# Kernel tuning notes

Measured on AMD Instinct MI355X. Metric: run time of the kernel, lower is better.

The kernel has to match this reference:

```python
import jax, jax.numpy as jnp
import numpy as np

ISIZE, REC, NACT, BS = 512, 1024, 18, 64
CLIPVAL = 2.0

def setup_inputs() -> dict:
    key = jax.random.key(0)
    ks = jax.random.split(key, 12)
    return {
        "inputs": jax.random.normal(ks[0], (BS, ISIZE), jnp.float32),
        "recurrent_vals": jax.random.normal(ks[1], (BS, REC), jnp.float32),
        "hebb": jax.random.normal(ks[2], (BS, REC, REC), jnp.float32) * 0.1,
        # plastic params
        "w": 0.001 * jax.random.uniform(ks[3], (REC, REC), jnp.float32),
        "alpha": 0.001 * jax.random.uniform(ks[4], (REC, REC), jnp.float32),
        # layer 0: Linear(isize, rec)
        "W0": jax.random.normal(ks[5], (REC, ISIZE), jnp.float32) / np.sqrt(ISIZE),
        "b0": jnp.zeros((REC,), jnp.float32),
        # layer 1: Linear(rec, NBACTIONS)
        "W1": jax.random.normal(ks[6], (NACT, REC), jnp.float32) / np.sqrt(REC),
        "b1": jnp.zeros((NACT,), jnp.float32),
        # h2mod: Linear(rec, 1)
        "h2mod_w": jax.random.normal(ks[7], (1, REC), jnp.float32) / np.sqrt(REC),
        "h2mod_b": jnp.zeros((1,), jnp.float32),
        # modfanout: Linear(1, rec)
        "modfanout_w": jax.random.normal(ks[8], (REC, 1), jnp.float32),
        "modfanout_b": jnp.zeros((REC,), jnp.float32),
    }


def reference(inputs, recurrent_vals, hebb, w, alpha, W0, b0, W1, b1,
              h2mod_w, h2mod_b, modfanout_w, modfanout_b):
    # recurrent layer (i == rec_layer_in == 0):
    # tanh(Linear0(x) + rv @ (w + alpha*hebb))  with per-batch plastic weights
    plastic = w[None, :, :] + alpha[None, :, :] * hebb          # [b, rec, rec]
    rec_in = jnp.einsum('bi,bij->bj', recurrent_vals, plastic)  # [b, rec]
    hactiv = jnp.tanh(inputs @ W0.T + b0 + rec_in)              # [b, rec]
    rec_layer_values = hactiv                                   # i == rec_layer_out
    logits = hactiv @ W1.T + b1                                 # [b, nact]
    act_dis = jax.nn.softmax(logits, axis=1)                    # sf=True
    # neuromodulation
    myeta = jnp.tanh(rec_layer_values @ h2mod_w.T + h2mod_b)    # [b, 1]
    eta = myeta[:, :, None] * modfanout_w.reshape(1, 1, REC) + modfanout_b  # [b,1,rec]
    deltahebb = recurrent_vals[:, :, None] * rec_layer_values[:, None, :]   # [b,rec,rec]
    hebb_return = jnp.clip(hebb + eta * deltahebb, -CLIPVAL, CLIPVAL)
    return act_dis, rec_layer_values, hebb_return
```

## Files before the change

### kernel.cpp

```cpp
#include <hip/hip_runtime.h>
#include <cmath>

constexpr int ISIZE = 512;
constexpr int REC   = 1024;
constexpr int NACT  = 18;
constexpr int BS    = 64;
constexpr float CLIPVAL = 2.0f;

constexpr int NSLOT = 17;


typedef float f4 __attribute__((ext_vector_type(4)));

__device__ __forceinline__ f4 nt_load(const f4* p) {
#if __has_builtin(__builtin_nontemporal_load)
  return __builtin_nontemporal_load(p);
#else
  return *p;
#endif
}
__device__ __forceinline__ void nt_store(f4* p, f4 v) {
#if __has_builtin(__builtin_nontemporal_store)
  __builtin_nontemporal_store(v, p);
#else
  *p = v;
#endif
}

__global__ __launch_bounds__(256) void k_pass1(
    const float* __restrict__ rv, const float* __restrict__ hebb,
    const float* __restrict__ w, const float* __restrict__ alpha,
    const float* __restrict__ x, const float* __restrict__ W0,
    float* __restrict__ part) {
  const int id = blockIdx.x;
  const int t  = threadIdx.x;

  if (id < 512) {
    const int bg = id & 15;
    const int jh = (id >> 4) & 1;
    const int ic = id >> 5;
    const int b0 = bg * 4, i0 = ic * 64;
    const int jl = t & 127, bl = t >> 7;
    const int j0 = jh * 512 + jl * 4;
    const int ba = b0 + bl * 2;

    __shared__ float rvs[4][64];
    rvs[t >> 6][t & 63] = rv[(size_t)(b0 + (t >> 6)) * REC + i0 + (t & 63)];
    __syncthreads();

    f4 a0 = {0.f, 0.f, 0.f, 0.f}, a1 = {0.f, 0.f, 0.f, 0.f};
    const float* __restrict__ wp  = w     + (size_t)i0 * REC + j0;
    const float* __restrict__ ap  = alpha + (size_t)i0 * REC + j0;
    const float* __restrict__ hp0 = hebb + ((size_t)ba * REC + i0) * REC + j0;
    const float* __restrict__ hp1 = hp0 + (size_t)REC * REC;
    const float* __restrict__ r0s = &rvs[bl * 2][0];
    const float* __restrict__ r1s = &rvs[bl * 2 + 1][0];

#pragma unroll 4
    for (int ii = 0; ii < 64; ++ii) {
      const f4 wv = *(const f4*)(wp  + (size_t)ii * REC);
      const f4 av = *(const f4*)(ap  + (size_t)ii * REC);
      const f4 h0 = *(const f4*)(hp0 + (size_t)ii * REC);
      const f4 h1 = *(const f4*)(hp1 + (size_t)ii * REC);
      const float r0 = r0s[ii], r1 = r1s[ii];
      a0.x = fmaf(r0, fmaf(av.x, h0.x, wv.x), a0.x);
      a0.y = fmaf(r0, fmaf(av.y, h0.y, wv.y), a0.y);
      a0.z = fmaf(r0, fmaf(av.z, h0.z, wv.z), a0.z);
      a0.w = fmaf(r0, fmaf(av.w, h0.w, wv.w), a0.w);
      a1.x = fmaf(r1, fmaf(av.x, h1.x, wv.x), a1.x);
      a1.y = fmaf(r1, fmaf(av.y, h1.y, wv.y), a1.y);
      a1.z = fmaf(r1, fmaf(av.z, h1.z, wv.z), a1.z);
      a1.w = fmaf(r1, fmaf(av.w, h1.w, wv.w), a1.w);
    }
    *(f4*)(part + ((size_t)ba * NSLOT + ic) * REC + j0)       = a0;
    *(f4*)(part + ((size_t)(ba + 1) * NSLOT + ic) * REC + j0) = a1;

  } else {
    const int idx = id - 512;
    const int jt = idx & 31, bg2 = idx >> 5;
    const int J0 = jt * 32, B0 = bg2 * 32;
    const int tx = t & 31, ty = t >> 5;
    __shared__ float w0s[32][33];
    __shared__ float xs[32][33];
    float acc[4] = {0.f, 0.f, 0.f, 0.f};
    for (int kk = 0; kk < ISIZE; kk += 32) {
#pragma unroll
      for (int r = 0; r < 32; r += 8) {
        w0s[tx][ty + r] = W0[(size_t)(J0 + ty + r) * ISIZE + kk + tx];
        xs[ty + r][tx]  = x [(size_t)(B0 + ty + r) * ISIZE + kk + tx];
      }
      __syncthreads();
#pragma unroll
      for (int k = 0; k < 32; ++k) {
        const float w0v = w0s[k][tx];
#pragma unroll
        for (int q = 0; q < 4; ++q)
          acc[q] = fmaf(xs[ty * 4 + q][k], w0v, acc[q]);
      }
      __syncthreads();
    }
#pragma unroll
    for (int q = 0; q < 4; ++q)
      part[((size_t)(B0 + ty * 4 + q) * NSLOT + 16) * REC + J0 + tx] = acc[q];
  }
}

__global__ __launch_bounds__(1024) void k_head(
    const float* __restrict__ part, const float* __restrict__ b0,
    const float* __restrict__ W1, const float* __restrict__ b1,
    const float* __restrict__ h2w, const float* __restrict__ h2b,
    const float* __restrict__ mw, const float* __restrict__ mb,
    float* __restrict__ hact, float* __restrict__ act_dis,
    float* __restrict__ g) {
  const int b = blockIdx.x;
  const int t = threadIdx.x;
  __shared__ float hsh[REC];
  __shared__ float logits_s[32];
  __shared__ float myeta_s;

  float s = b0[t];
  const float* __restrict__ pb = part + (size_t)b * NSLOT * REC + t;
#pragma unroll
  for (int sl = 0; sl < NSLOT; ++sl) s += pb[(size_t)sl * REC];
  const float h = tanhf(s);
  hact[(size_t)b * REC + t] = h;
  hsh[t] = h;
  __syncthreads();

  const int wv = t >> 6, ln = t & 63;
  for (int a = wv; a < NACT; a += 16) {
    const float* __restrict__ w1a = W1 + (size_t)a * REC;
    float p = 0.f;
#pragma unroll
    for (int c = 0; c < 16; ++c) p = fmaf(hsh[c * 64 + ln], w1a[c * 64 + ln], p);
#pragma unroll
    for (int off = 32; off; off >>= 1) p += __shfl_down(p, off);
    if (ln == 0) logits_s[a] = p + b1[a];
  }
  if (wv == 0) {
    float p = 0.f;
#pragma unroll
    for (int c = 0; c < 16; ++c) p = fmaf(hsh[c * 64 + ln], h2w[c * 64 + ln], p);
#pragma unroll
    for (int off = 32; off; off >>= 1) p += __shfl_down(p, off);
    if (ln == 0) myeta_s = tanhf(p + h2b[0]);
  }
  __syncthreads();

  if (t == 0) {
    float m = logits_s[0];
    for (int a = 1; a < NACT; ++a) m = fmaxf(m, logits_s[a]);
    float e[NACT];
    float ssum = 0.f;
    for (int a = 0; a < NACT; ++a) { e[a] = expf(logits_s[a] - m); ssum += e[a]; }
    const float inv = 1.f / ssum;
    for (int a = 0; a < NACT; ++a) act_dis[(size_t)b * NACT + a] = e[a] * inv;
  }

  const float me = myeta_s;
  g[(size_t)b * REC + t] = fmaf(me, mw[t], mb[t]) * hsh[t];
}

__global__ __launch_bounds__(256) void k_hebb(
    const float* __restrict__ hebb, const float* __restrict__ rv,
    const float* __restrict__ g, float* __restrict__ out) {
  const int b  = 63 - (int)blockIdx.x;
  const int i0 = (127 - (int)blockIdx.y) * 8;
  const int j0 = threadIdx.x * 4;
  const f4 gv = *(const f4*)(g + (size_t)b * REC + j0);
  const float* __restrict__ rvb = rv + (size_t)b * REC;
  const size_t base = ((size_t)b * REC + i0) * REC + j0;
#pragma unroll
  for (int ii = 0; ii < 8; ++ii) {
    const float r = rvb[i0 + ii];
    const f4 hv = nt_load((const f4*)(hebb + base + (size_t)ii * REC));
    f4 o;
    o.x = fminf(fmaxf(fmaf(r, gv.x, hv.x), -CLIPVAL), CLIPVAL);
    o.y = fminf(fmaxf(fmaf(r, gv.y, hv.y), -CLIPVAL), CLIPVAL);
    o.z = fminf(fmaxf(fmaf(r, gv.z, hv.z), -CLIPVAL), CLIPVAL);
    o.w = fminf(fmaxf(fmaf(r, gv.w, hv.w), -CLIPVAL), CLIPVAL);
    nt_store((f4*)(out + base + (size_t)ii * REC), o);
  }
}

extern "C" void kernel_launch(void* const* d_in, const int* in_sizes, int n_in,
                              void* d_out, int out_size, void* d_ws, size_t ws_size,
                              hipStream_t stream) {
  const float* x     = (const float*)d_in[0];
  const float* rv    = (const float*)d_in[1];
  const float* hebb  = (const float*)d_in[2];
  const float* w     = (const float*)d_in[3];
  const float* alpha = (const float*)d_in[4];
  const float* W0    = (const float*)d_in[5];
  const float* b0    = (const float*)d_in[6];
  const float* W1    = (const float*)d_in[7];
  const float* b1    = (const float*)d_in[8];
  const float* h2w   = (const float*)d_in[9];
  const float* h2b   = (const float*)d_in[10];
  const float* mw    = (const float*)d_in[11];
  const float* mb    = (const float*)d_in[12];

  float* out_act  = (float*)d_out;
  float* out_hact = out_act + (size_t)BS * NACT;
  float* out_hebb = out_hact + (size_t)BS * REC;

  float* part = (float*)d_ws;
  float* g    = part + (size_t)BS * NSLOT * REC;

  k_pass1<<<576, 256, 0, stream>>>(rv, hebb, w, alpha, x, W0, part);
  k_head<<<BS, 1024, 0, stream>>>(part, b0, W1, b1, h2w, h2b, mw, mb,
                                  out_hact, out_act, g);
  k_hebb<<<dim3(64, 128), 256, 0, stream>>>(hebb, rv, g, out_hebb);
}
```

Baseline: 155.5 us.

## Fuse three kernels into one cooperative kernel with grid syncs

Replaces the three-kernel sequence (plastic matvec pass, head, hebb update) with one cooperative kernel that uses two grid-wide syncs. After the second sync, the blocks that read hebb in the first phase re-read the same hebb tiles for the update, hoping to hit in cache, and they reuse the rv values already held in shared memory. This removes two launch gaps. The cost is grid syncs, a head phase that runs on only 64 blocks while the rest wait, and a dependence on all 576 blocks being co-resident. If the cooperative launch fails, the code falls back to the original three kernels.

```diff
diff --git a/kernel.cpp b/kernel.cpp
--- a/kernel.cpp
+++ b/kernel.cpp
@@ -1,14 +1,15 @@
 #include <hip/hip_runtime.h>
+#include <hip/hip_cooperative_groups.h>
 #include <cmath>
+
+namespace cg = cooperative_groups;
 
 constexpr int ISIZE = 512;
 constexpr int REC   = 1024;
 constexpr int NACT  = 18;
 constexpr int BS    = 64;
 constexpr float CLIPVAL = 2.0f;
-
 constexpr int NSLOT = 17;
-
 
 typedef float f4 __attribute__((ext_vector_type(4)));
 
@@ -27,25 +28,37 @@
 #endif
 }
 
-__global__ __launch_bounds__(256) void k_pass1(
+__global__ __launch_bounds__(256, 3) void k_fused(
     const float* __restrict__ rv, const float* __restrict__ hebb,
     const float* __restrict__ w, const float* __restrict__ alpha,
     const float* __restrict__ x, const float* __restrict__ W0,
-    float* __restrict__ part) {
+    const float* __restrict__ b0, const float* __restrict__ W1,
+    const float* __restrict__ b1, const float* __restrict__ h2w,
+    const float* __restrict__ h2b, const float* __restrict__ mw,
+    const float* __restrict__ mb, float* __restrict__ part,
+    float* __restrict__ g, float* __restrict__ hact,
+    float* __restrict__ act_dis, float* __restrict__ out) {
+  cg::grid_group grid = cg::this_grid();
   const int id = blockIdx.x;
   const int t  = threadIdx.x;
+
+  __shared__ float rvs[4][64];
+  __shared__ float w0s[32][33];
+  __shared__ float xs2[32][33];
+  __shared__ float hsh[REC];
+  __shared__ float logits_s[32];
+  __shared__ float myeta_s;
 
   if (id < 512) {
     const int bg = id & 15;
     const int jh = (id >> 4) & 1;
     const int ic = id >> 5;
-    const int b0 = bg * 4, i0 = ic * 64;
+    const int b0i = bg * 4, i0 = ic * 64;
     const int jl = t & 127, bl = t >> 7;
     const int j0 = jh * 512 + jl * 4;
-    const int ba = b0 + bl * 2;
-
-    __shared__ float rvs[4][64];
-    rvs[t >> 6][t & 63] = rv[(size_t)(b0 + (t >> 6)) * REC + i0 + (t & 63)];
+    const int ba = b0i + bl * 2;
+
+    rvs[t >> 6][t & 63] = rv[(size_t)(b0i + (t >> 6)) * REC + i0 + (t & 63)];
     __syncthreads();
 
     f4 a0 = {0.f, 0.f, 0.f, 0.f}, a1 = {0.f, 0.f, 0.f, 0.f};
@@ -74,7 +87,177 @@
     }
     *(f4*)(part + ((size_t)ba * NSLOT + ic) * REC + j0)       = a0;
     *(f4*)(part + ((size_t)(ba + 1) * NSLOT + ic) * REC + j0) = a1;
-
+  } else {
+    const int idx = id - 512;
+    const int jt = idx & 31, bg2 = idx >> 5;
+    const int J0 = jt * 32, B0 = bg2 * 32;
+    const int tx = t & 31, ty = t >> 5;
+    float acc[4] = {0.f, 0.f, 0.f, 0.f};
+    for (int kk = 0; kk < ISIZE; kk += 32) {
+#pragma unroll
+      for (int r = 0; r < 32; r += 8) {
+        w0s[tx][ty + r] = W0[(size_t)(J0 + ty + r) * ISIZE + kk + tx];
+        xs2[ty + r][tx] = x [(size_t)(B0 + ty + r) * ISIZE + kk + tx];
+      }
+      __syncthreads();
+#pragma unroll
+      for (int k = 0; k < 32; ++k) {
+        const float w0v = w0s[k][tx];
+#pragma unroll
+        for (int q = 0; q < 4; ++q)
+          acc[q] = fmaf(xs2[ty * 4 + q][k], w0v, acc[q]);
+      }
+      __syncthreads();
+    }
+#pragma unroll
+    for (int q = 0; q < 4; ++q)
+      part[((size_t)(B0 + ty * 4 + q) * NSLOT + 16) * REC + J0 + tx] = acc[q];
+  }
+
+  __threadfence();
+  grid.sync();
+
+  if (id < BS) {
+    const int b = id;
+    const int j0 = t * 4;
+
+    f4 s = *(const f4*)(b0 + j0);
+#pragma unroll
+    for (int sl = 0; sl < NSLOT; ++sl) {
+      const f4 p = *(const f4*)(part + ((size_t)b * NSLOT + sl) * REC + j0);
+      s.x += p.x; s.y += p.y; s.z += p.z; s.w += p.w;
+    }
+    f4 h4;
+    h4.x = tanhf(s.x); h4.y = tanhf(s.y); h4.z = tanhf(s.z); h4.w = tanhf(s.w);
+    *(f4*)(hact + (size_t)b * REC + j0) = h4;
+    *(f4*)(&hsh[j0]) = h4;
+    __syncthreads();
+
+    const int wid = t >> 6, ln = t & 63;
+    for (int a = wid; a < NACT; a += 4) {
+      const float* __restrict__ w1a = W1 + (size_t)a * REC;
+      float p = 0.f;
+#pragma unroll
+      for (int c = 0; c < 16; ++c) p = fmaf(hsh[c * 64 + ln], w1a[c * 64 + ln], p);
+#pragma unroll
+      for (int off = 32; off; off >>= 1) p += __shfl_down(p, off);
+      if (ln == 0) logits_s[a] = p + b1[a];
+    }
+    if (wid == 3) {
+      float p = 0.f;
+#pragma unroll
+      for (int c = 0; c < 16; ++c) p = fmaf(hsh[c * 64 + ln], h2w[c * 64 + ln], p);
+#pragma unroll
+      for (int off = 32; off; off >>= 1) p += __shfl_down(p, off);
+      if (ln == 0) myeta_s = tanhf(p + h2b[0]);
+    }
+    __syncthreads();
+
+    if (t == 0) {
+      float m = logits_s[0];
+      for (int a = 1; a < NACT; ++a) m = fmaxf(m, logits_s[a]);
+      float e[NACT];
+      float ssum = 0.f;
+      for (int a = 0; a < NACT; ++a) { e[a] = expf(logits_s[a] - m); ssum += e[a]; }
+      const float inv = 1.f / ssum;
+      for (int a = 0; a < NACT; ++a) act_dis[(size_t)b * NACT + a] = e[a] * inv;
+    }
+    __syncthreads();
+
+    const float me = myeta_s;
+    const f4 mwv = *(const f4*)(mw + j0);
+    const f4 mbv = *(const f4*)(mb + j0);
+    const f4 hh  = *(const f4*)(&hsh[j0]);
+    f4 gv;
+    gv.x = fmaf(me, mwv.x, mbv.x) * hh.x;
+    gv.y = fmaf(me, mwv.y, mbv.y) * hh.y;
+    gv.z = fmaf(me, mwv.z, mbv.z) * hh.z;
+    gv.w = fmaf(me, mwv.w, mbv.w) * hh.w;
+    *(f4*)(g + (size_t)b * REC + j0) = gv;
+  }
+
+  __threadfence();
+  grid.sync();
+
+  if (id < 512) {
+    const int bg = id & 15;
+    const int jh = (id >> 4) & 1;
+    const int ic = id >> 5;
+    const int b0i = bg * 4, i0 = ic * 64;
+    const int jl = t & 127, bl = t >> 7;
+    const int j0 = jh * 512 + jl * 4;
+    const int ba = b0i + bl * 2;
+
+    const f4 g0 = *(const f4*)(g + (size_t)ba * REC + j0);
+    const f4 g1 = *(const f4*)(g + (size_t)(ba + 1) * REC + j0);
+    const float* __restrict__ r0s = &rvs[bl * 2][0];
+    const float* __restrict__ r1s = &rvs[bl * 2 + 1][0];
+    const float* __restrict__ hp0 = hebb + ((size_t)ba * REC + i0) * REC + j0;
+    const float* __restrict__ hp1 = hp0 + (size_t)REC * REC;
+    float* __restrict__ op0 = out + ((size_t)ba * REC + i0) * REC + j0;
+    float* __restrict__ op1 = op0 + (size_t)REC * REC;
+
+#pragma unroll 4
+    for (int ii = 0; ii < 64; ++ii) {
+      const f4 h0 = *(const f4*)(hp0 + (size_t)ii * REC);
+      const f4 h1 = *(const f4*)(hp1 + (size_t)ii * REC);
+      const float r0 = r0s[ii], r1 = r1s[ii];
+      f4 o0, o1;
+      o0.x = fminf(fmaxf(fmaf(r0, g0.x, h0.x), -CLIPVAL), CLIPVAL);
+      o0.y = fminf(fmaxf(fmaf(r0, g0.y, h0.y), -CLIPVAL), CLIPVAL);
+      o0.z = fminf(fmaxf(fmaf(r0, g0.z, h0.z), -CLIPVAL), CLIPVAL);
+      o0.w = fminf(fmaxf(fmaf(r0, g0.w, h0.w), -CLIPVAL), CLIPVAL);
+      o1.x = fminf(fmaxf(fmaf(r1, g1.x, h1.x), -CLIPVAL), CLIPVAL);
+      o1.y = fminf(fmaxf(fmaf(r1, g1.y, h1.y), -CLIPVAL), CLIPVAL);
+      o1.z = fminf(fmaxf(fmaf(r1, g1.z, h1.z), -CLIPVAL), CLIPVAL);
+      o1.w = fminf(fmaxf(fmaf(r1, g1.w, h1.w), -CLIPVAL), CLIPVAL);
+      nt_store((f4*)(op0 + (size_t)ii * REC), o0);
+      nt_store((f4*)(op1 + (size_t)ii * REC), o1);
+    }
+  }
+}
+
+__global__ __launch_bounds__(256) void k_pass1_fb(
+    const float* __restrict__ rv, const float* __restrict__ hebb,
+    const float* __restrict__ w, const float* __restrict__ alpha,
+    const float* __restrict__ x, const float* __restrict__ W0,
+    float* __restrict__ part) {
+  const int id = blockIdx.x;
+  const int t  = threadIdx.x;
+  if (id < 512) {
+    const int bg = id & 15;
+    const int jh = (id >> 4) & 1;
+    const int ic = id >> 5;
+    const int b0 = bg * 4, i0 = ic * 64;
+    const int jl = t & 127, bl = t >> 7;
+    const int j0 = jh * 512 + jl * 4;
+    const int ba = b0 + bl * 2;
+    __shared__ float rvs[4][64];
+    rvs[t >> 6][t & 63] = rv[(size_t)(b0 + (t >> 6)) * REC + i0 + (t & 63)];
+    __syncthreads();
+    f4 a0 = {0.f, 0.f, 0.f, 0.f}, a1 = {0.f, 0.f, 0.f, 0.f};
+    const float* __restrict__ wp  = w     + (size_t)i0 * REC + j0;
+    const float* __restrict__ ap  = alpha + (size_t)i0 * REC + j0;
+    const float* __restrict__ hp0 = hebb + ((size_t)ba * REC + i0) * REC + j0;
+    const float* __restrict__ hp1 = hp0 + (size_t)REC * REC;
+#pragma unroll 4
+    for (int ii = 0; ii < 64; ++ii) {
+      const f4 wv = *(const f4*)(wp  + (size_t)ii * REC);
+      const f4 av = *(const f4*)(ap  + (size_t)ii * REC);
+      const f4 h0 = *(const f4*)(hp0 + (size_t)ii * REC);
+      const f4 h1 = *(const f4*)(hp1 + (size_t)ii * REC);
+      const float r0 = rvs[bl * 2][ii], r1 = rvs[bl * 2 + 1][ii];
+      a0.x = fmaf(r0, fmaf(av.x, h0.x, wv.x), a0.x);
+      a0.y = fmaf(r0, fmaf(av.y, h0.y, wv.y), a0.y);
+      a0.z = fmaf(r0, fmaf(av.z, h0.z, wv.z), a0.z);
+      a0.w = fmaf(r0, fmaf(av.w, h0.w, wv.w), a0.w);
+      a1.x = fmaf(r1, fmaf(av.x, h1.x, wv.x), a1.x);
+      a1.y = fmaf(r1, fmaf(av.y, h1.y, wv.y), a1.y);
+      a1.z = fmaf(r1, fmaf(av.z, h1.z, wv.z), a1.z);
+      a1.w = fmaf(r1, fmaf(av.w, h1.w, wv.w), a1.w);
+    }
+    *(f4*)(part + ((size_t)ba * NSLOT + ic) * REC + j0)       = a0;
+    *(f4*)(part + ((size_t)(ba + 1) * NSLOT + ic) * REC + j0) = a1;
   } else {
     const int idx = id - 512;
     const int jt = idx & 31, bg2 = idx >> 5;
@@ -105,7 +288,7 @@
   }
 }
 
-__global__ __launch_bounds__(1024) void k_head(
+__global__ __launch_bounds__(1024) void k_head_fb(
     const float* __restrict__ part, const float* __restrict__ b0,
     const float* __restrict__ W1, const float* __restrict__ b1,
     const float* __restrict__ h2w, const float* __restrict__ h2b,
@@ -117,7 +300,6 @@
   __shared__ float hsh[REC];
   __shared__ float logits_s[32];
   __shared__ float myeta_s;
-
   float s = b0[t];
   const float* __restrict__ pb = part + (size_t)b * NSLOT * REC + t;
 #pragma unroll
@@ -126,7 +308,6 @@
   hact[(size_t)b * REC + t] = h;
   hsh[t] = h;
   __syncthreads();
-
   const int wv = t >> 6, ln = t & 63;
   for (int a = wv; a < NACT; a += 16) {
     const float* __restrict__ w1a = W1 + (size_t)a * REC;
@@ -146,7 +327,6 @@
     if (ln == 0) myeta_s = tanhf(p + h2b[0]);
   }
   __syncthreads();
-
   if (t == 0) {
     float m = logits_s[0];
     for (int a = 1; a < NACT; ++a) m = fmaxf(m, logits_s[a]);
@@ -156,12 +336,12 @@
     const float inv = 1.f / ssum;
     for (int a = 0; a < NACT; ++a) act_dis[(size_t)b * NACT + a] = e[a] * inv;
   }
-
+  __syncthreads();
   const float me = myeta_s;
   g[(size_t)b * REC + t] = fmaf(me, mw[t], mb[t]) * hsh[t];
 }
 
-__global__ __launch_bounds__(256) void k_hebb(
+__global__ __launch_bounds__(256) void k_hebb_fb(
     const float* __restrict__ hebb, const float* __restrict__ rv,
     const float* __restrict__ g, float* __restrict__ out) {
   const int b  = 63 - (int)blockIdx.x;
@@ -207,8 +387,17 @@
   float* part = (float*)d_ws;
   float* g    = part + (size_t)BS * NSLOT * REC;
 
-  k_pass1<<<576, 256, 0, stream>>>(rv, hebb, w, alpha, x, W0, part);
-  k_head<<<BS, 1024, 0, stream>>>(part, b0, W1, b1, h2w, h2b, mw, mb,
-                                  out_hact, out_act, g);
-  k_hebb<<<dim3(64, 128), 256, 0, stream>>>(hebb, rv, g, out_hebb);
-}
+  void* args[] = {(void*)&rv,  (void*)&hebb, (void*)&w,   (void*)&alpha,
+                  (void*)&x,   (void*)&W0,   (void*)&b0,  (void*)&W1,
+                  (void*)&b1,  (void*)&h2w,  (void*)&h2b, (void*)&mw,
+                  (void*)&mb,  (void*)&part, (void*)&g,   (void*)&out_hact,
+                  (void*)&out_act, (void*)&out_hebb};
+  hipError_t err = hipLaunchCooperativeKernel(k_fused, dim3(576), dim3(256),
+                                              args, 0, stream);
+  if (err != hipSuccess) {
+    k_pass1_fb<<<576, 256, 0, stream>>>(rv, hebb, w, alpha, x, W0, part);
+    k_head_fb<<<BS, 1024, 0, stream>>>(part, b0, W1, b1, h2w, h2b, mw, mb,
+                                       out_hact, out_act, g);
+    k_hebb_fb<<<dim3(64, 128), 256, 0, stream>>>(hebb, rv, g, out_hebb);
+  }
+}
```

Result: slower. 411.8 us (+164.9%).

## Split batch into two groups so hebb reread hits the cache

Applied to the files above, without the earlier changes.

Runs the pass1/head/hebb pipeline twice, once per half of the batch (32 items), so each group's hebb slice (128MB) may still sit in the last-level cache when k_hebb rereads it. The k_hebb load becomes a normal cached load instead of nontemporal, and the block order runs forward rather than reversed. Launch count doubles and each launch has fewer blocks, which could cut occupancy. A __syncthreads before reading myeta_s is also added.

```diff
diff --git a/kernel.cpp b/kernel.cpp
--- a/kernel.cpp
+++ b/kernel.cpp
@@ -6,19 +6,12 @@
 constexpr int NACT  = 18;
 constexpr int BS    = 64;
 constexpr float CLIPVAL = 2.0f;
-
 constexpr int NSLOT = 17;
-
+constexpr int GB    = 32;
+constexpr int NGR   = BS / GB;
 
 typedef float f4 __attribute__((ext_vector_type(4)));
 
-__device__ __forceinline__ f4 nt_load(const f4* p) {
-#if __has_builtin(__builtin_nontemporal_load)
-  return __builtin_nontemporal_load(p);
-#else
-  return *p;
-#endif
-}
 __device__ __forceinline__ void nt_store(f4* p, f4 v) {
 #if __has_builtin(__builtin_nontemporal_store)
   __builtin_nontemporal_store(v, p);
@@ -31,21 +24,21 @@
     const float* __restrict__ rv, const float* __restrict__ hebb,
     const float* __restrict__ w, const float* __restrict__ alpha,
     const float* __restrict__ x, const float* __restrict__ W0,
-    float* __restrict__ part) {
+    float* __restrict__ part, int gbase) {
   const int id = blockIdx.x;
   const int t  = threadIdx.x;
 
-  if (id < 512) {
-    const int bg = id & 15;
-    const int jh = (id >> 4) & 1;
-    const int ic = id >> 5;
-    const int b0 = bg * 4, i0 = ic * 64;
+  if (id < 256) {
+    const int bg = id & 7;
+    const int jh = (id >> 3) & 1;
+    const int ic = id >> 4;
+    const int b0i = gbase + bg * 4, i0 = ic * 64;
     const int jl = t & 127, bl = t >> 7;
     const int j0 = jh * 512 + jl * 4;
-    const int ba = b0 + bl * 2;
+    const int ba = b0i + bl * 2;
 
     __shared__ float rvs[4][64];
-    rvs[t >> 6][t & 63] = rv[(size_t)(b0 + (t >> 6)) * REC + i0 + (t & 63)];
+    rvs[t >> 6][t & 63] = rv[(size_t)(b0i + (t >> 6)) * REC + i0 + (t & 63)];
     __syncthreads();
 
     f4 a0 = {0.f, 0.f, 0.f, 0.f}, a1 = {0.f, 0.f, 0.f, 0.f};
@@ -76,9 +69,8 @@
     *(f4*)(part + ((size_t)(ba + 1) * NSLOT + ic) * REC + j0) = a1;
 
   } else {
-    const int idx = id - 512;
-    const int jt = idx & 31, bg2 = idx >> 5;
-    const int J0 = jt * 32, B0 = bg2 * 32;
+    const int jt = id - 256;
+    const int J0 = jt * 32, B0 = gbase;
     const int tx = t & 31, ty = t >> 5;
     __shared__ float w0s[32][33];
     __shared__ float xs[32][33];
@@ -111,8 +103,8 @@
     const float* __restrict__ h2w, const float* __restrict__ h2b,
     const float* __restrict__ mw, const float* __restrict__ mb,
     float* __restrict__ hact, float* __restrict__ act_dis,
-    float* __restrict__ g) {
-  const int b = blockIdx.x;
+    float* __restrict__ g, int gbase) {
+  const int b = gbase + blockIdx.x;
   const int t = threadIdx.x;
   __shared__ float hsh[REC];
   __shared__ float logits_s[32];
@@ -156,16 +148,16 @@
     const float inv = 1.f / ssum;
     for (int a = 0; a < NACT; ++a) act_dis[(size_t)b * NACT + a] = e[a] * inv;
   }
-
+  __syncthreads();
   const float me = myeta_s;
   g[(size_t)b * REC + t] = fmaf(me, mw[t], mb[t]) * hsh[t];
 }
 
 __global__ __launch_bounds__(256) void k_hebb(
     const float* __restrict__ hebb, const float* __restrict__ rv,
-    const float* __restrict__ g, float* __restrict__ out) {
-  const int b  = 63 - (int)blockIdx.x;
-  const int i0 = (127 - (int)blockIdx.y) * 8;
+    const float* __restrict__ g, float* __restrict__ out, int gbase) {
+  const int b  = gbase + blockIdx.x;
+  const int i0 = blockIdx.y * 8;
   const int j0 = threadIdx.x * 4;
   const f4 gv = *(const f4*)(g + (size_t)b * REC + j0);
   const float* __restrict__ rvb = rv + (size_t)b * REC;
@@ -173,7 +165,7 @@
 #pragma unroll
   for (int ii = 0; ii < 8; ++ii) {
     const float r = rvb[i0 + ii];
-    const f4 hv = nt_load((const f4*)(hebb + base + (size_t)ii * REC));
+    const f4 hv = *(const f4*)(hebb + base + (size_t)ii * REC);
     f4 o;
     o.x = fminf(fmaxf(fmaf(r, gv.x, hv.x), -CLIPVAL), CLIPVAL);
     o.y = fminf(fmaxf(fmaf(r, gv.y, hv.y), -CLIPVAL), CLIPVAL);
@@ -207,8 +199,11 @@
   float* part = (float*)d_ws;
   float* g    = part + (size_t)BS * NSLOT * REC;
 
-  k_pass1<<<576, 256, 0, stream>>>(rv, hebb, w, alpha, x, W0, part);
-  k_head<<<BS, 1024, 0, stream>>>(part, b0, W1, b1, h2w, h2b, mw, mb,
-                                  out_hact, out_act, g);
-  k_hebb<<<dim3(64, 128), 256, 0, stream>>>(hebb, rv, g, out_hebb);
-}
+  for (int grp = 0; grp < NGR; ++grp) {
+    const int gbase = grp * GB;
+    k_pass1<<<288, 256, 0, stream>>>(rv, hebb, w, alpha, x, W0, part, gbase);
+    k_head<<<GB, 1024, 0, stream>>>(part, b0, W1, b1, h2w, h2b, mw, mb,
+                                    out_hact, out_act, g, gbase);
+    k_hebb<<<dim3(GB, 128), 256, 0, stream>>>(hebb, rv, g, out_hebb, gbase);
+  }
+}
```

Measured after the change: 164.6 us. 1.06x slower.

## Fuse head and hebb update into persistent work-queue kernel with per-batch flags

Applied to the files above, without the earlier changes.

Replaces the separate head and hebb-update kernels with one persistent kernel that pulls jobs from an atomic counter. The first 64 jobs compute the per-batch head (tanh, logits, softmax, modulation vector g) and publish a release flag. The remaining 1024 jobs each update a 64-row hebb slab and spin on the flag for their batch. This removes one launch boundary and lets the hebb streaming overlap the head computation. In exchange it adds a memset, atomics and spin-waits, and the hebb loads change from nontemporal to normal loads.

```diff
diff --git a/kernel.cpp b/kernel.cpp
--- a/kernel.cpp
+++ b/kernel.cpp
@@ -6,19 +6,10 @@
 constexpr int NACT  = 18;
 constexpr int BS    = 64;
 constexpr float CLIPVAL = 2.0f;
-
 constexpr int NSLOT = 17;
 
-
 typedef float f4 __attribute__((ext_vector_type(4)));
 
-__device__ __forceinline__ f4 nt_load(const f4* p) {
-#if __has_builtin(__builtin_nontemporal_load)
-  return __builtin_nontemporal_load(p);
-#else
-  return *p;
-#endif
-}
 __device__ __forceinline__ void nt_store(f4* p, f4 v) {
 #if __has_builtin(__builtin_nontemporal_store)
   __builtin_nontemporal_store(v, p);
@@ -39,13 +30,13 @@
     const int bg = id & 15;
     const int jh = (id >> 4) & 1;
     const int ic = id >> 5;
-    const int b0 = bg * 4, i0 = ic * 64;
+    const int b0i = bg * 4, i0 = ic * 64;
     const int jl = t & 127, bl = t >> 7;
     const int j0 = jh * 512 + jl * 4;
-    const int ba = b0 + bl * 2;
+    const int ba = b0i + bl * 2;
 
     __shared__ float rvs[4][64];
-    rvs[t >> 6][t & 63] = rv[(size_t)(b0 + (t >> 6)) * REC + i0 + (t & 63)];
+    rvs[t >> 6][t & 63] = rv[(size_t)(b0i + (t >> 6)) * REC + i0 + (t & 63)];
     __syncthreads();
 
     f4 a0 = {0.f, 0.f, 0.f, 0.f}, a1 = {0.f, 0.f, 0.f, 0.f};
@@ -105,81 +96,130 @@
   }
 }
 
-__global__ __launch_bounds__(1024) void k_head(
-    const float* __restrict__ part, const float* __restrict__ b0,
-    const float* __restrict__ W1, const float* __restrict__ b1,
-    const float* __restrict__ h2w, const float* __restrict__ h2b,
-    const float* __restrict__ mw, const float* __restrict__ mb,
-    float* __restrict__ hact, float* __restrict__ act_dis,
-    float* __restrict__ g) {
-  const int b = blockIdx.x;
+constexpr int NJOBS2 = 64 + 1024;
+
+__global__ __launch_bounds__(256, 2) void k_tail(
+    const float* __restrict__ rv,  const float* __restrict__ hebb,
+    const float* __restrict__ b0,  const float* __restrict__ W1,
+    const float* __restrict__ b1,  const float* __restrict__ h2w,
+    const float* __restrict__ h2b, const float* __restrict__ mw,
+    const float* __restrict__ mb,  const float* __restrict__ part,
+    float* __restrict__ g,         int* __restrict__ sync,
+    float* __restrict__ hact,      float* __restrict__ act_dis,
+    float* __restrict__ out) {
   const int t = threadIdx.x;
+  __shared__ int s_job;
   __shared__ float hsh[REC];
   __shared__ float logits_s[32];
   __shared__ float myeta_s;
 
-  float s = b0[t];
-  const float* __restrict__ pb = part + (size_t)b * NSLOT * REC + t;
-#pragma unroll
-  for (int sl = 0; sl < NSLOT; ++sl) s += pb[(size_t)sl * REC];
-  const float h = tanhf(s);
-  hact[(size_t)b * REC + t] = h;
-  hsh[t] = h;
-  __syncthreads();
-
-  const int wv = t >> 6, ln = t & 63;
-  for (int a = wv; a < NACT; a += 16) {
-    const float* __restrict__ w1a = W1 + (size_t)a * REC;
-    float p = 0.f;
-#pragma unroll
-    for (int c = 0; c < 16; ++c) p = fmaf(hsh[c * 64 + ln], w1a[c * 64 + ln], p);
-#pragma unroll
-    for (int off = 32; off; off >>= 1) p += __shfl_down(p, off);
-    if (ln == 0) logits_s[a] = p + b1[a];
-  }
-  if (wv == 0) {
-    float p = 0.f;
-#pragma unroll
-    for (int c = 0; c < 16; ++c) p = fmaf(hsh[c * 64 + ln], h2w[c * 64 + ln], p);
-#pragma unroll
-    for (int off = 32; off; off >>= 1) p += __shfl_down(p, off);
-    if (ln == 0) myeta_s = tanhf(p + h2b[0]);
-  }
-  __syncthreads();
-
-  if (t == 0) {
-    float m = logits_s[0];
-    for (int a = 1; a < NACT; ++a) m = fmaxf(m, logits_s[a]);
-    float e[NACT];
-    float ssum = 0.f;
-    for (int a = 0; a < NACT; ++a) { e[a] = expf(logits_s[a] - m); ssum += e[a]; }
-    const float inv = 1.f / ssum;
-    for (int a = 0; a < NACT; ++a) act_dis[(size_t)b * NACT + a] = e[a] * inv;
-  }
-
-  const float me = myeta_s;
-  g[(size_t)b * REC + t] = fmaf(me, mw[t], mb[t]) * hsh[t];
-}
-
-__global__ __launch_bounds__(256) void k_hebb(
-    const float* __restrict__ hebb, const float* __restrict__ rv,
-    const float* __restrict__ g, float* __restrict__ out) {
-  const int b  = 63 - (int)blockIdx.x;
-  const int i0 = (127 - (int)blockIdx.y) * 8;
-  const int j0 = threadIdx.x * 4;
-  const f4 gv = *(const f4*)(g + (size_t)b * REC + j0);
-  const float* __restrict__ rvb = rv + (size_t)b * REC;
-  const size_t base = ((size_t)b * REC + i0) * REC + j0;
-#pragma unroll
-  for (int ii = 0; ii < 8; ++ii) {
-    const float r = rvb[i0 + ii];
-    const f4 hv = nt_load((const f4*)(hebb + base + (size_t)ii * REC));
-    f4 o;
-    o.x = fminf(fmaxf(fmaf(r, gv.x, hv.x), -CLIPVAL), CLIPVAL);
-    o.y = fminf(fmaxf(fmaf(r, gv.y, hv.y), -CLIPVAL), CLIPVAL);
-    o.z = fminf(fmaxf(fmaf(r, gv.z, hv.z), -CLIPVAL), CLIPVAL);
-    o.w = fminf(fmaxf(fmaf(r, gv.w, hv.w), -CLIPVAL), CLIPVAL);
-    nt_store((f4*)(out + base + (size_t)ii * REC), o);
+  for (;;) {
+    __syncthreads();
+    if (t == 0) s_job = atomicAdd(&sync[0], 1);
+    __syncthreads();
+    const int j = s_job;
+    if (j >= NJOBS2) return;
+
+    if (j < 64) {
+      const int b  = 63 - j;
+      const int j0 = t * 4;
+
+      f4 s = *(const f4*)(b0 + j0);
+#pragma unroll
+      for (int sl = 0; sl < NSLOT; ++sl) {
+        const f4 p = *(const f4*)(part + ((size_t)b * NSLOT + sl) * REC + j0);
+        s.x += p.x; s.y += p.y; s.z += p.z; s.w += p.w;
+      }
+      f4 h4;
+      h4.x = tanhf(s.x); h4.y = tanhf(s.y); h4.z = tanhf(s.z); h4.w = tanhf(s.w);
+      *(f4*)(hact + (size_t)b * REC + j0) = h4;
+      *(f4*)(&hsh[j0]) = h4;
+      __syncthreads();
+
+      const int wid = t >> 6, ln = t & 63;
+      for (int a = wid; a < NACT; a += 4) {
+        const float* __restrict__ w1a = W1 + (size_t)a * REC;
+        float p = 0.f;
+#pragma unroll
+        for (int c = 0; c < 16; ++c) p = fmaf(hsh[c * 64 + ln], w1a[c * 64 + ln], p);
+#pragma unroll
+        for (int off = 32; off; off >>= 1) p += __shfl_down(p, off);
+        if (ln == 0) logits_s[a] = p + b1[a];
+      }
+      if (wid == 3) {
+        float p = 0.f;
+#pragma unroll
+        for (int c = 0; c < 16; ++c) p = fmaf(hsh[c * 64 + ln], h2w[c * 64 + ln], p);
+#pragma unroll
+        for (int off = 32; off; off >>= 1) p += __shfl_down(p, off);
+        if (ln == 0) myeta_s = tanhf(p + h2b[0]);
+      }
+      __syncthreads();
+
+      if (t == 0) {
+        float m = logits_s[0];
+        for (int a = 1; a < NACT; ++a) m = fmaxf(m, logits_s[a]);
+        float e[NACT];
+        float ssum = 0.f;
+        for (int a = 0; a < NACT; ++a) { e[a] = expf(logits_s[a] - m); ssum += e[a]; }
+        const float inv = 1.f / ssum;
+        for (int a = 0; a < NACT; ++a) act_dis[(size_t)b * NACT + a] = e[a] * inv;
+      }
+      __syncthreads();
+
+      const float me = myeta_s;
+      const f4 mwv = *(const f4*)(mw + j0);
+      const f4 mbv = *(const f4*)(mb + j0);
+      const f4 hh  = *(const f4*)(&hsh[j0]);
+      f4 gv;
+      gv.x = fmaf(me, mwv.x, mbv.x) * hh.x;
+      gv.y = fmaf(me, mwv.y, mbv.y) * hh.y;
+      gv.z = fmaf(me, mwv.z, mbv.z) * hh.z;
+      gv.w = fmaf(me, mwv.w, mbv.w) * hh.w;
+      float* __restrict__ gb = g + (size_t)b * REC + j0;
+      __hip_atomic_store(&gb[0], gv.x, __ATOMIC_RELAXED, __HIP_MEMORY_SCOPE_AGENT);
+      __hip_atomic_store(&gb[1], gv.y, __ATOMIC_RELAXED, __HIP_MEMORY_SCOPE_AGENT);
+      __hip_atomic_store(&gb[2], gv.z, __ATOMIC_RELAXED, __HIP_MEMORY_SCOPE_AGENT);
+      __hip_atomic_store(&gb[3], gv.w, __ATOMIC_RELAXED, __HIP_MEMORY_SCOPE_AGENT);
+      __syncthreads();
+      if (t == 0)
+        __hip_atomic_store(&sync[1 + b], 1, __ATOMIC_RELEASE, __HIP_MEMORY_SCOPE_AGENT);
+
+    } else {
+      const int r  = j - 64;
+      const int ic = 15 - (r >> 6);
+      const int b  = 63 - (r & 63);
+      const int i0 = ic * 64;
+      const int j0 = t * 4;
+
+      if (t == 0) {
+        while (__hip_atomic_load(&sync[1 + b], __ATOMIC_ACQUIRE,
+                                 __HIP_MEMORY_SCOPE_AGENT) == 0)
+          __builtin_amdgcn_s_sleep(8);
+      }
+      __syncthreads();
+
+      const float* __restrict__ gb = g + (size_t)b * REC + j0;
+      f4 gv;
+      gv.x = __hip_atomic_load(&gb[0], __ATOMIC_RELAXED, __HIP_MEMORY_SCOPE_AGENT);
+      gv.y = __hip_atomic_load(&gb[1], __ATOMIC_RELAXED, __HIP_MEMORY_SCOPE_AGENT);
+      gv.z = __hip_atomic_load(&gb[2], __ATOMIC_RELAXED, __HIP_MEMORY_SCOPE_AGENT);
+      gv.w = __hip_atomic_load(&gb[3], __ATOMIC_RELAXED, __HIP_MEMORY_SCOPE_AGENT);
+
+      const float* __restrict__ rvb = rv + (size_t)b * REC + i0;
+      const size_t base = ((size_t)b * REC + i0) * REC + j0;
+#pragma unroll 4
+      for (int ii = 0; ii < 64; ++ii) {
+        const float rr = rvb[ii];
+        const f4 hv = *(const f4*)(hebb + base + (size_t)ii * REC);
+        f4 o;
+        o.x = fminf(fmaxf(fmaf(rr, gv.x, hv.x), -CLIPVAL), CLIPVAL);
+        o.y = fminf(fmaxf(fmaf(rr, gv.y, hv.y), -CLIPVAL), CLIPVAL);
+        o.z = fminf(fmaxf(fmaf(rr, gv.z, hv.z), -CLIPVAL), CLIPVAL);
+        o.w = fminf(fmaxf(fmaf(rr, gv.w, hv.w), -CLIPVAL), CLIPVAL);
+        nt_store((f4*)(out + base + (size_t)ii * REC), o);
+      }
+    }
   }
 }
 
@@ -206,9 +246,10 @@
 
   float* part = (float*)d_ws;
   float* g    = part + (size_t)BS * NSLOT * REC;
-
+  int*   sync = (int*)(g + (size_t)BS * REC);
+
+  hipMemsetAsync(sync, 0, (1 + BS) * sizeof(int), stream);
   k_pass1<<<576, 256, 0, stream>>>(rv, hebb, w, alpha, x, W0, part);
-  k_head<<<BS, 1024, 0, stream>>>(part, b0, W1, b1, h2w, h2b, mw, mb,
-                                  out_hact, out_act, g);
-  k_hebb<<<dim3(64, 128), 256, 0, stream>>>(hebb, rv, g, out_hebb);
-}
+  k_tail<<<512, 256, 0, stream>>>(rv, hebb, b0, W1, b1, h2w, h2b, mw, mb,
+                                  part, g, sync, out_hact, out_act, out_hebb);
+}
```

After: 213.2 us. +37.1%, slower.
